# Kernel optimization log

Measured on AMD Instinct MI355X. Metric: run time of the kernel, lower is better.

The kernel has to match this reference:

```python
import jax, jax.numpy as jnp
import numpy as np

B, A, NN, G, F, L, MAXZ = 8, 1024, 64, 25, 128, 3, 100
CUTOFF = 5.0

def ssp(x):
    # shifted softplus: ln(0.5*e^x + 0.5) = softplus(x) - ln(2)
    return jax.nn.softplus(x) - jnp.log(2.0)

def setup_inputs() -> dict:
    key = jax.random.key(0)
    ks = jax.random.split(key, 10)
    atomic_numbers = jax.random.randint(ks[0], (B, A), 0, MAXZ)
    positions = jax.random.normal(ks[1], (B, A, 3), dtype=jnp.float32) * 3.0
    cell = jnp.zeros((B, 3, 3), dtype=jnp.float32)
    cell_offset = jnp.zeros((B, A, NN, 3), dtype=jnp.float32)
    neighbors = jax.random.randint(ks[2], (B, A, NN), 0, A)
    neighbor_mask = jnp.ones((B, A, NN), dtype=jnp.float32)
    s = 0.05
    emb = jax.random.normal(ks[3], (MAXZ, F), dtype=jnp.float32) * s
    emb = emb.at[0].set(0.0)  # padding_idx=0
    return dict(
        atomic_numbers=atomic_numbers, positions=positions, cell=cell,
        cell_offset=cell_offset, neighbors=neighbors, neighbor_mask=neighbor_mask,
        emb=emb,
        fw1=jax.random.normal(ks[4], (L, G, F), dtype=jnp.float32) * s,
        fb1=jnp.zeros((L, F), dtype=jnp.float32),
        fw2=jax.random.normal(ks[5], (L, F, F), dtype=jnp.float32) * s,
        fb2=jnp.zeros((L, F), dtype=jnp.float32),
        in2f_w=jax.random.normal(ks[6], (L, F, F), dtype=jnp.float32) * s,
        f2out_w=jax.random.normal(ks[7], (L, F, F), dtype=jnp.float32) * s,
        f2out_b=jnp.zeros((L, F), dtype=jnp.float32),
        dense_w=jax.random.normal(ks[8], (L, F, F), dtype=jnp.float32) * s,
        dense_b=jnp.zeros((L, F), dtype=jnp.float32),
    )

def reference(atomic_numbers, positions, cell, cell_offset, neighbors,
              neighbor_mask, emb, fw1, fb1, fw2, fb2, in2f_w, f2out_w,
              f2out_b, dense_w, dense_b):
    bidx = jnp.arange(B)[:, None, None]
    # embedding lookup [B,A,F]
    x = emb[atomic_numbers]
    # AtomDistances: gather neighbor positions, add cell offsets, norm
    pos_j = positions[bidx, neighbors]                       # [B,A,NN,3]
    dv = pos_j - positions[:, :, None, :] + jnp.einsum('bank,bkc->banc', cell_offset, cell)
    d2 = jnp.sum(dv * dv, axis=-1)                           # [B,A,NN]
    r_ij = jnp.where(d2 > 0, jnp.sqrt(jnp.where(d2 > 0, d2, 1.0)), 0.0)
    # GaussianSmearing on [0, cutoff] with G gaussians
    offsets = jnp.linspace(0.0, CUTOFF, G)
    width = offsets[1] - offsets[0]
    coeff = -0.5 / (width * width)
    f_ij = jnp.exp(coeff * (r_ij[..., None] - offsets) ** 2)  # [B,A,NN,G]
    mask = neighbor_mask[..., None]                           # [B,A,NN,1]
    for l in range(L):
        # filter-generating network on expanded distances -> [B,A,NN,F]
        W = ssp(f_ij @ fw1[l] + fb1[l]) @ fw2[l] + fb2[l]
        # cfconv: in2f (no bias), gather neighbor features, mul, masked sum
        y = x @ in2f_w[l]                                     # [B,A,F]
        yj = y[bidx, neighbors]                               # [B,A,NN,F]
        v = jnp.sum(yj * W * mask, axis=2)                    # [B,A,F]
        v = ssp(v @ f2out_w[l] + f2out_b[l])
        # interaction output dense (linear)
        v = v @ dense_w[l] + dense_b[l]
        x = x + v
    return x
```

## Files before the change

kernel.cpp:

```cpp
#include <hip/hip_runtime.h>
#include <hip/hip_bf16.h>
#include <math.h>

#define B_ 8
#define A_ 1024
#define NN_ 64
#define G_ 25
#define F_ 128
#define L_ 3
#define TG_ 4096
#define TGP_ (TG_ + 8)
#define SCT 32.0f
#define SCY 64.0f
#define INVS (1.0f/(32.0f*64.0f))

typedef __hip_bfloat16 bf16;
typedef __bf16 bf16x8 __attribute__((ext_vector_type(8)));
typedef __bf16 bf16x4 __attribute__((ext_vector_type(4)));
typedef float floatx4 __attribute__((ext_vector_type(4)));
typedef float floatx2 __attribute__((ext_vector_type(2)));
#define MFMA16 __builtin_amdgcn_mfma_f32_16x16x32_bf16
#define CVT8 __builtin_amdgcn_cvt_pk_f32_fp8

__device__ __forceinline__ float sspfast(float x){
  return __logf(0.5f*__expf(x) + 0.5f);
}
__device__ __forceinline__ float ldsel(const void* p, long long i, int isbf){
  return isbf ? __bfloat162float(((const bf16*)p)[i]) : ((const float*)p)[i];
}
__device__ __forceinline__ int sniff_bf16(const void* pos){
  const unsigned* raw = (const unsigned*)pos;
  unsigned w = raw[threadIdx.x & 63];
  unsigned e = (w >> 7) & 0xFF;
  return __popcll(__ballot(e >= 118 && e <= 132)) >= 32;
}
__device__ __forceinline__ unsigned int pack4_fp8(float a, float b, float c, float d){
  int r = __builtin_amdgcn_cvt_pk_fp8_f32(a, b, 0, false);
  r = __builtin_amdgcn_cvt_pk_fp8_f32(c, d, r, true);
  return (unsigned int)r;
}

__global__ __launch_bounds__(256) void k_setup(
    const void* emb, const void* fb1, const void* fb2, const void* f2ob,
    const void* db,  const void* fw1, const void* fw2, const void* f2ow,
    const void* dw,  const void* in2f, const void* pos,
    float* c_emb, float* c_fb1, float* c_fb2, float* c_f2ob, float* c_db,
    __bf16* fw1tb, __bf16* fw2tb, __bf16* f2owtb, __bf16* dwtb, __bf16* in2ftb)
{
  int isbf = sniff_bf16(pos);
  int idx = blockIdx.x*256 + threadIdx.x;
  if(idx < 12800){ c_emb[idx] = ldsel(emb, idx, isbf); return; }
  if(idx < 13184){ c_fb1[idx-12800] = ldsel(fb1, idx-12800, isbf); return; }
  if(idx < 13568){ c_fb2[idx-13184] = ldsel(fb2, idx-13184, isbf); return; }
  if(idx < 13952){ c_f2ob[idx-13568] = ldsel(f2ob, idx-13568, isbf); return; }
  if(idx < 14336){ c_db[idx-13952] = ldsel(db, idx-13952, isbf); return; }
  if(idx < 26624){
    int i = idx - 14336;
    int l = i >> 12; int rem = i & 4095; int f = rem >> 5; int k = rem & 31;
    float v = (k < G_) ? ldsel(fw1, (long long)l*G_*F_ + k*F_ + f, isbf) : 0.0f;
    fw1tb[i] = (__bf16)v;
    return;
  }
  {
    int i = idx - 26624;
    int which = i / 49152; int r = i - which*49152;
    int l = r >> 14; int rem = r & 16383; int f = rem >> 7; int k = rem & 127;
    const void* src = (which==0) ? fw2 : (which==1) ? f2ow : (which==2) ? dw : in2f;
    __bf16* dst = (which==0) ? fw2tb : (which==1) ? f2owtb : (which==2) ? dwtb : in2ftb;
    dst[r] = (__bf16)ldsel(src, (long long)l*F_*F_ + k*F_ + f, isbf);
  }
}

__global__ __launch_bounds__(256, 4) void k_build(
    const __bf16* __restrict__ fw1tb, const float* __restrict__ fb1g,
    const __bf16* __restrict__ fw2tb, const float* __restrict__ fb2g,
    unsigned char* __restrict__ wtab8,
    const int* __restrict__ z, const float* __restrict__ c_emb,
    const __bf16* __restrict__ in2ftb, float* __restrict__ xws,
    unsigned char* __restrict__ y8,
    const void* pos, const void* cell, const void* celloff,
    const int* __restrict__ nbr, const void* maskg,
    int2* __restrict__ pair)
{
  __shared__ __align__(16) unsigned char smem[22528];
  int t = threadIdx.x;
  int lane = t & 63, wid = t >> 6, c = lane & 15, quad = lane >> 4;
  int wb = wid*32;

  if(blockIdx.x >= 448){
    int isbf = sniff_bf16(pos);
    int p = (blockIdx.x - 448)*256 + t;
    int m = p >> 6;
    int b = m >> 10;
    int j = nbr[p];
    long long pi = (long long)m*3, pj = (long long)(b*A_+j)*3;
    long long co = (long long)p*3, ce = (long long)b*9;
    float o0 = ldsel(celloff,co+0,isbf), o1 = ldsel(celloff,co+1,isbf), o2 = ldsel(celloff,co+2,isbf);
    float d2 = 0.0f;
    #pragma unroll
    for(int cc=0;cc<3;cc++){
      float off = o0*ldsel(cell,ce+cc,isbf) + o1*ldsel(cell,ce+3+cc,isbf) + o2*ldsel(cell,ce+6+cc,isbf);
      float dv = ldsel(pos,pj+cc,isbf) - ldsel(pos,pi+cc,isbf) + off;
      d2 += dv*dv;
    }
    float r = (d2 > 0.0f) ? sqrtf(d2) : 0.0f;
    float msk = ldsel(maskg, p, isbf);
    int i = (int)(r * ((float)TG_ / 8.0f) + 0.5f);
    if(i > TG_-1) i = TG_-1;
    if(msk < 0.5f) i = TG_;
    int2 pr;
    pr.x = i * F_;
    pr.y = (b*A_ + j) * F_;
    pair[p] = pr;
    return;
  }

  if(blockIdx.x < 192){
    __bf16* s_h1  = (__bf16*)smem;
    __bf16* s_fij = (__bf16*)(smem + 17408);
    int layer = blockIdx.x >> 6;
    int row0  = (blockIdx.x & 63) * 64;
    unsigned char* T8 = wtab8 + (long long)layer*TGP_*F_;

    if((blockIdx.x & 63) == 0 && t < 32)
      *(unsigned int*)(T8 + (long long)TG_*F_ + t*4) = 0u;

    const float dr = 8.0f / (float)TG_;
    const float width = 5.0f/24.0f;
    const float coeff = -0.5f/(width*width);
    for(int i=t;i<NN_*40;i+=256){
      int n = i/40, g = i - n*40;
      float val = 0.0f;
      if(g < G_){
        float rg = (float)(row0 + n) * dr;
        float d = rg - (float)g*width;
        val = __expf(coeff*d*d);
      }
      s_fij[i] = (__bf16)val;
    }
    __syncthreads();

    {
      const __bf16* fw1l = fw1tb + layer*F_*32;
      bf16x8 a0 = *(const bf16x8*)(fw1l + (wb + c)*32 + quad*8);
      bf16x8 a1 = *(const bf16x8*)(fw1l + (wb + 16 + c)*32 + quad*8);
      floatx4 bias0 = *(const floatx4*)(fb1g + layer*F_ + wb + quad*4);
      floatx4 bias1 = *(const floatx4*)(fb1g + layer*F_ + wb + 16 + quad*4);
      #pragma unroll
      for(int nt=0;nt<4;nt++){
        bf16x8 bfr = *(const bf16x8*)(s_fij + (nt*16 + c)*40 + quad*8);
        floatx4 z4 = {0.f,0.f,0.f,0.f};
        floatx4 acc0 = MFMA16(a0, bfr, z4, 0,0,0);
        floatx4 acc1 = MFMA16(a1, bfr, z4, 0,0,0);
        bf16x4 h0, h1v;
        #pragma unroll
        for(int r=0;r<4;r++){
          h0[r]  = (__bf16)sspfast(acc0[r] + bias0[r]);
          h1v[r] = (__bf16)sspfast(acc1[r] + bias1[r]);
        }
        *(bf16x4*)(s_h1 + (nt*16+c)*136 + wb + quad*4)      = h0;
        *(bf16x4*)(s_h1 + (nt*16+c)*136 + wb + 16 + quad*4) = h1v;
      }
    }
    __syncthreads();

    {
      const __bf16* fw2l = fw2tb + layer*F_*F_;
      bf16x8 aw0[4], aw1[4];
      #pragma unroll
      for(int kt=0;kt<4;kt++){
        aw0[kt] = *(const bf16x8*)(fw2l + (wb + c)*F_ + kt*32 + quad*8);
        aw1[kt] = *(const bf16x8*)(fw2l + (wb + 16 + c)*F_ + kt*32 + quad*8);
      }
      floatx4 ba0 = *(const floatx4*)(fb2g + layer*F_ + wb + quad*4);
      floatx4 ba1 = *(const floatx4*)(fb2g + layer*F_ + wb + 16 + quad*4);
      #pragma unroll
      for(int nt=0; nt<4; nt++){
        bf16x8 bh[4];
        #pragma unroll
        for(int kt=0;kt<4;kt++)
          bh[kt] = *(const bf16x8*)(s_h1 + (nt*16 + c)*136 + kt*32 + quad*8);
        floatx4 acc0 = {0.f,0.f,0.f,0.f};
        floatx4 acc1 = {0.f,0.f,0.f,0.f};
        #pragma unroll
        for(int kt=0;kt<4;kt++){
          acc0 = MFMA16(aw0[kt], bh[kt], acc0, 0,0,0);
          acc1 = MFMA16(aw1[kt], bh[kt], acc1, 0,0,0);
        }
        int row = row0 + nt*16 + c;
        unsigned int w0 = pack4_fp8((acc0[0]+ba0[0])*SCT, (acc0[1]+ba0[1])*SCT,
                                    (acc0[2]+ba0[2])*SCT, (acc0[3]+ba0[3])*SCT);
        unsigned int w1 = pack4_fp8((acc1[0]+ba1[0])*SCT, (acc1[1]+ba1[1])*SCT,
                                    (acc1[2]+ba1[2])*SCT, (acc1[3]+ba1[3])*SCT);
        *(unsigned int*)(T8 + (long long)row*F_ + wb + quad*4)      = w0;
        *(unsigned int*)(T8 + (long long)row*F_ + wb + 16 + quad*4) = w1;
      }
    }
    return;
  }

  {
    __bf16* s_a = (__bf16*)smem;
    int row0 = (blockIdx.x - 192)*32;
    #pragma unroll
    for(int i=0;i<2;i++){
      int ch = t + i*256, row = ch >> 4, col8 = ch & 15;
      const float* src = c_emb + (long long)z[row0+row]*F_ + col8*8;
      float4 a4 = ((const float4*)src)[0];
      float4 b4 = ((const float4*)src)[1];
      float* xd = xws + (long long)(row0+row)*F_ + col8*8;
      ((float4*)xd)[0] = a4; ((float4*)xd)[1] = b4;
      bf16x8 v = {(__bf16)a4.x,(__bf16)a4.y,(__bf16)a4.z,(__bf16)a4.w,
                  (__bf16)b4.x,(__bf16)b4.y,(__bf16)b4.z,(__bf16)b4.w};
      *(bf16x8*)(s_a + row*136 + col8*8) = v;
    }
    __syncthreads();
    bf16x8 aw0[4], aw1[4];
    #pragma unroll
    for(int kt=0;kt<4;kt++){
      aw0[kt] = *(const bf16x8*)(in2ftb + (wb + c)*F_ + kt*32 + quad*8);
      aw1[kt] = *(const bf16x8*)(in2ftb + (wb + 16 + c)*F_ + kt*32 + quad*8);
    }
    #pragma unroll
    for(int nt=0; nt<2; nt++){
      bf16x8 bh[4];
      #pragma unroll
      for(int kt=0;kt<4;kt++)
        bh[kt] = *(const bf16x8*)(s_a + (nt*16 + c)*136 + kt*32 + quad*8);
      floatx4 acc0 = {0.f,0.f,0.f,0.f};
      floatx4 acc1 = {0.f,0.f,0.f,0.f};
      #pragma unroll
      for(int kt=0;kt<4;kt++){
        acc0 = MFMA16(aw0[kt], bh[kt], acc0, 0,0,0);
        acc1 = MFMA16(aw1[kt], bh[kt], acc1, 0,0,0);
      }
      int row = row0 + nt*16 + c;
      unsigned int w0 = pack4_fp8(acc0[0]*SCY, acc0[1]*SCY, acc0[2]*SCY, acc0[3]*SCY);
      unsigned int w1 = pack4_fp8(acc1[0]*SCY, acc1[1]*SCY, acc1[2]*SCY, acc1[3]*SCY);
      *(unsigned int*)(y8 + (long long)row*F_ + wb + quad*4)      = w0;
      *(unsigned int*)(y8 + (long long)row*F_ + wb + 16 + quad*4) = w1;
    }
  }
}

__global__ __launch_bounds__(512, 4) void k_layer(
    const unsigned char* __restrict__ yin, const int2* __restrict__ pairg,
    const unsigned char* __restrict__ Tb, float* __restrict__ xws,
    const __bf16* __restrict__ f2owl, const float* __restrict__ f2obl,
    const __bf16* __restrict__ dwl,  const float* __restrict__ dbl,
    const __bf16* __restrict__ in2fnext, unsigned char* __restrict__ yout,
    void* __restrict__ dout, const void* __restrict__ pos,
    int has_next, int write_out)
{
  __shared__ __align__(16) __bf16 s_ga[16*136];
  __shared__ __align__(16) __bf16 s_gb[16*136];

  int t = threadIdx.x;
  int bid = (int)blockIdx.x;
  int m0 = ((bid & 7) * 64 + (bid >> 3)) * 16;
  int lane = t & 63, wid = t >> 6, c = lane & 15, quad = lane >> 4;
  int isbf = sniff_bf16(pos);
  int wb = wid*16;

  int fs  = lane & 7;
  int grp = lane >> 3;
  int f16 = fs*16;

  const int2* pbase = pairg + (long long)m0*NN_;
  int2 prs0[8], prs1[8];
  {
    int a0 = wid*2, a1 = wid*2 + 1;
    #pragma unroll
    for(int jj=0; jj<8; jj++){
      prs0[jj] = pbase[a0*NN_ + jj*8 + grp];
      prs1[jj] = pbase[a1*NN_ + jj*8 + grp];
    }
  }

  #pragma unroll
  for(int aa=0; aa<2; aa++){
    int a = wid*2 + aa;
    float v0=0.f,v1=0.f,v2=0.f,v3=0.f,v4=0.f,v5=0.f,v6=0.f,v7=0.f;
    float v8=0.f,v9=0.f,v10=0.f,v11=0.f,v12=0.f,v13=0.f,v14=0.f,v15=0.f;
    #pragma unroll
    for(int jj=0; jj<8; jj++){
      int2 pr = aa ? prs1[jj] : prs0[jj];
      uint4 Tw = *(const uint4*)(Tb + pr.x + f16);
      uint4 Yw = *(const uint4*)(yin + pr.y + f16);
      floatx2 ta0 = CVT8((int)Tw.x,false), ta1 = CVT8((int)Tw.x,true);
      floatx2 ta2 = CVT8((int)Tw.y,false), ta3 = CVT8((int)Tw.y,true);
      floatx2 ta4 = CVT8((int)Tw.z,false), ta5 = CVT8((int)Tw.z,true);
      floatx2 ta6 = CVT8((int)Tw.w,false), ta7 = CVT8((int)Tw.w,true);
      floatx2 ua0 = CVT8((int)Yw.x,false), ua1 = CVT8((int)Yw.x,true);
      floatx2 ua2 = CVT8((int)Yw.y,false), ua3 = CVT8((int)Yw.y,true);
      floatx2 ua4 = CVT8((int)Yw.z,false), ua5 = CVT8((int)Yw.z,true);
      floatx2 ua6 = CVT8((int)Yw.w,false), ua7 = CVT8((int)Yw.w,true);
      v0  += ta0[0]*ua0[0];  v1  += ta0[1]*ua0[1];
      v2  += ta1[0]*ua1[0];  v3  += ta1[1]*ua1[1];
      v4  += ta2[0]*ua2[0];  v5  += ta2[1]*ua2[1];
      v6  += ta3[0]*ua3[0];  v7  += ta3[1]*ua3[1];
      v8  += ta4[0]*ua4[0];  v9  += ta4[1]*ua4[1];
      v10 += ta5[0]*ua5[0];  v11 += ta5[1]*ua5[1];
      v12 += ta6[0]*ua6[0];  v13 += ta6[1]*ua6[1];
      v14 += ta7[0]*ua7[0];  v15 += ta7[1]*ua7[1];
    }
    #define RED(m) \
      v0 += __shfl_xor(v0,m);  v1 += __shfl_xor(v1,m);  v2 += __shfl_xor(v2,m);  v3 += __shfl_xor(v3,m); \
      v4 += __shfl_xor(v4,m);  v5 += __shfl_xor(v5,m);  v6 += __shfl_xor(v6,m);  v7 += __shfl_xor(v7,m); \
      v8 += __shfl_xor(v8,m);  v9 += __shfl_xor(v9,m);  v10 += __shfl_xor(v10,m); v11 += __shfl_xor(v11,m); \
      v12 += __shfl_xor(v12,m); v13 += __shfl_xor(v13,m); v14 += __shfl_xor(v14,m); v15 += __shfl_xor(v15,m);
    RED(8) RED(16) RED(32)
    #undef RED
    if(lane < 8){
      bf16x8 o0 = {(__bf16)(v0*INVS),(__bf16)(v1*INVS),(__bf16)(v2*INVS),(__bf16)(v3*INVS),
                   (__bf16)(v4*INVS),(__bf16)(v5*INVS),(__bf16)(v6*INVS),(__bf16)(v7*INVS)};
      bf16x8 o1 = {(__bf16)(v8*INVS),(__bf16)(v9*INVS),(__bf16)(v10*INVS),(__bf16)(v11*INVS),
                   (__bf16)(v12*INVS),(__bf16)(v13*INVS),(__bf16)(v14*INVS),(__bf16)(v15*INVS)};
      *(bf16x8*)(s_ga + a*136 + fs*16)     = o0;
      *(bf16x8*)(s_ga + a*136 + fs*16 + 8) = o1;
    }
  }
  __syncthreads();

  {
    bf16x8 aw[4];
    #pragma unroll
    for(int kt=0;kt<4;kt++)
      aw[kt] = *(const bf16x8*)(f2owl + (wb + c)*F_ + kt*32 + quad*8);
    floatx4 ba = *(const floatx4*)(f2obl + wb + quad*4);
    bf16x8 bh[4];
    #pragma unroll
    for(int kt=0;kt<4;kt++)
      bh[kt] = *(const bf16x8*)(s_ga + c*136 + kt*32 + quad*8);
    floatx4 acc = {0.f,0.f,0.f,0.f};
    #pragma unroll
    for(int kt=0;kt<4;kt++)
      acc = MFMA16(aw[kt], bh[kt], acc, 0,0,0);
    bf16x4 o;
    #pragma unroll
    for(int r=0;r<4;r++)
      o[r] = (__bf16)sspfast(acc[r] + ba[r]);
    *(bf16x4*)(s_gb + c*136 + wb + quad*4) = o;
  }
  __syncthreads();

  {
    bf16x8 aw[4];
    #pragma unroll
    for(int kt=0;kt<4;kt++)
      aw[kt] = *(const bf16x8*)(dwl + (wb + c)*F_ + kt*32 + quad*8);
    floatx4 ba = *(const floatx4*)(dbl + wb + quad*4);
    bf16x8 bh[4];
    #pragma unroll
    for(int kt=0;kt<4;kt++)
      bh[kt] = *(const bf16x8*)(s_gb + c*136 + kt*32 + quad*8);
    floatx4 acc = {0.f,0.f,0.f,0.f};
    #pragma unroll
    for(int kt=0;kt<4;kt++)
      acc = MFMA16(aw[kt], bh[kt], acc, 0,0,0);
    int rowL = m0 + c;
    float* xp = xws + (long long)rowL*F_ + wb + quad*4;
    float4 x0 = *(const float4*)xp;
    float4 xn = {x0.x+acc[0]+ba[0], x0.y+acc[1]+ba[1],
                 x0.z+acc[2]+ba[2], x0.w+acc[3]+ba[3]};
    bf16x4 s0 = {(__bf16)xn.x,(__bf16)xn.y,(__bf16)xn.z,(__bf16)xn.w};
    *(bf16x4*)(s_ga + c*136 + wb + quad*4) = s0;
    *(float4*)xp = xn;
    if(write_out){
      long long gi = (long long)rowL*F_ + wb + quad*4;
      if(isbf){
        *(bf16x4*)((bf16*)dout + gi) = s0;
      }else{
        *(float4*)((float*)dout + gi) = xn;
      }
    }
  }
  if(!has_next) return;
  __syncthreads();

  {
    bf16x8 aw[4];
    #pragma unroll
    for(int kt=0;kt<4;kt++)
      aw[kt] = *(const bf16x8*)(in2fnext + (wb + c)*F_ + kt*32 + quad*8);
    bf16x8 bh[4];
    #pragma unroll
    for(int kt=0;kt<4;kt++)
      bh[kt] = *(const bf16x8*)(s_ga + c*136 + kt*32 + quad*8);
    floatx4 acc = {0.f,0.f,0.f,0.f};
    #pragma unroll
    for(int kt=0;kt<4;kt++)
      acc = MFMA16(aw[kt], bh[kt], acc, 0,0,0);
    int row = m0 + c;
    unsigned int w0 = pack4_fp8(acc[0]*SCY, acc[1]*SCY, acc[2]*SCY, acc[3]*SCY);
    *(unsigned int*)(yout + (long long)row*F_ + wb + quad*4) = w0;
  }
}

extern "C" void kernel_launch(void* const* d_in, const int* in_sizes, int n_in,
                              void* d_out, int out_size, void* d_ws, size_t ws_size,
                              hipStream_t stream){
  const int*  z       = (const int*)d_in[0];
  const void* pos     = d_in[1];
  const void* cell    = d_in[2];
  const void* celloff = d_in[3];
  const int*  nbr     = (const int*)d_in[4];
  const void* mask    = d_in[5];
  const void* emb     = d_in[6];
  const void* fw1     = d_in[7];
  const void* fb1     = d_in[8];
  const void* fw2     = d_in[9];
  const void* fb2     = d_in[10];
  const void* in2f    = d_in[11];
  const void* f2ow    = d_in[12];
  const void* f2ob    = d_in[13];
  const void* dw      = d_in[14];
  const void* db      = d_in[15];

  float* base = (float*)d_ws;
  float* c_emb  = base + 16;
  float* c_fb1  = c_emb + 12800;
  float* c_fb2  = c_fb1 + 384;
  float* c_f2ob = c_fb2 + 384;
  float* c_db   = c_f2ob + 384;
  __bf16* fw1tb  = (__bf16*)(c_db + 384);
  __bf16* fw2tb  = (__bf16*)(base + 20496);
  __bf16* f2owtb = (__bf16*)(base + 45072);
  __bf16* dwtb   = (__bf16*)(base + 69648);
  __bf16* in2ftb = (__bf16*)(base + 94224);
  float*  xws   = base + 118800;
  unsigned char* y8_0 = (unsigned char*)(base + 1167376);
  unsigned char* y8_1 = (unsigned char*)(base + 1429520);
  int2*   pair  = (int2*)(base + 1691664);
  unsigned char* wtab8 = (unsigned char*)(base + 2740240);

  k_setup<<<872, 256, 0, stream>>>(emb, fb1, fb2, f2ob, db,
                                   fw1, fw2, f2ow, dw, in2f, pos,
                                   c_emb, c_fb1, c_fb2, c_f2ob, c_db,
                                   fw1tb, fw2tb, f2owtb, dwtb, in2ftb);
  k_build<<<2496, 256, 0, stream>>>(fw1tb, c_fb1, fw2tb, c_fb2, wtab8,
                                    z, c_emb, in2ftb, xws, y8_0,
                                    pos, cell, celloff, nbr, mask, pair);

  unsigned char* ycur = y8_0;
  unsigned char* ynext = y8_1;
  for(int l=0;l<L_;l++){
    k_layer<<<(B_*A_)/16, 512, 0, stream>>>(ycur, pair,
                                            wtab8 + (long long)l*TGP_*F_, xws,
                                            f2owtb + l*F_*F_, c_f2ob + l*F_,
                                            dwtb + l*F_*F_,  c_db + l*F_,
                                            in2ftb + (l < L_-1 ? (l+1)*F_*F_ : 0), ynext,
                                            d_out, pos,
                                            (l < L_-1) ? 1 : 0, (l == L_-1) ? 1 : 0);
    unsigned char* tmp = ycur; ycur = ynext; ynext = tmp;
  }
}
```

Measured before the change: 155.2 us.

## Fold setup kernel into build kernel, reading raw weights directly

Removes the separate k_setup launch and moves its work into k_build. The table-build and embedding blocks now read fw1/fw2/fb/emb/in2f straight from the raw inputs with per-element dtype conversion, and new trailing blocks transpose f2ow/dw/in2f and copy the biases for the later layer kernels. Block order is rearranged so the pair-distance blocks come first. This removes one launch and its serialization, at the cost of uncoalesced strided scalar weight loads in each table/embedding block. The embedding-stage in2f load now reads raw layer-0 weights instead of the transposed buffer, which the fused kernel fills concurrently.

Result: slower. 169.0 us (+8.9%).

```diff
diff --git a/kernel.cpp b/kernel.cpp
--- a/kernel.cpp
+++ b/kernel.cpp
@@ -40,56 +40,27 @@
   return (unsigned int)r;
 }
 
-__global__ __launch_bounds__(256) void k_setup(
-    const void* emb, const void* fb1, const void* fb2, const void* f2ob,
-    const void* db,  const void* fw1, const void* fw2, const void* f2ow,
-    const void* dw,  const void* in2f, const void* pos,
-    float* c_emb, float* c_fb1, float* c_fb2, float* c_f2ob, float* c_db,
-    __bf16* fw1tb, __bf16* fw2tb, __bf16* f2owtb, __bf16* dwtb, __bf16* in2ftb)
-{
-  int isbf = sniff_bf16(pos);
-  int idx = blockIdx.x*256 + threadIdx.x;
-  if(idx < 12800){ c_emb[idx] = ldsel(emb, idx, isbf); return; }
-  if(idx < 13184){ c_fb1[idx-12800] = ldsel(fb1, idx-12800, isbf); return; }
-  if(idx < 13568){ c_fb2[idx-13184] = ldsel(fb2, idx-13184, isbf); return; }
-  if(idx < 13952){ c_f2ob[idx-13568] = ldsel(f2ob, idx-13568, isbf); return; }
-  if(idx < 14336){ c_db[idx-13952] = ldsel(db, idx-13952, isbf); return; }
-  if(idx < 26624){
-    int i = idx - 14336;
-    int l = i >> 12; int rem = i & 4095; int f = rem >> 5; int k = rem & 31;
-    float v = (k < G_) ? ldsel(fw1, (long long)l*G_*F_ + k*F_ + f, isbf) : 0.0f;
-    fw1tb[i] = (__bf16)v;
-    return;
-  }
-  {
-    int i = idx - 26624;
-    int which = i / 49152; int r = i - which*49152;
-    int l = r >> 14; int rem = r & 16383; int f = rem >> 7; int k = rem & 127;
-    const void* src = (which==0) ? fw2 : (which==1) ? f2ow : (which==2) ? dw : in2f;
-    __bf16* dst = (which==0) ? fw2tb : (which==1) ? f2owtb : (which==2) ? dwtb : in2ftb;
-    dst[r] = (__bf16)ldsel(src, (long long)l*F_*F_ + k*F_ + f, isbf);
-  }
-}
-
 __global__ __launch_bounds__(256, 4) void k_build(
-    const __bf16* __restrict__ fw1tb, const float* __restrict__ fb1g,
-    const __bf16* __restrict__ fw2tb, const float* __restrict__ fb2g,
-    unsigned char* __restrict__ wtab8,
-    const int* __restrict__ z, const float* __restrict__ c_emb,
-    const __bf16* __restrict__ in2ftb, float* __restrict__ xws,
-    unsigned char* __restrict__ y8,
     const void* pos, const void* cell, const void* celloff,
     const int* __restrict__ nbr, const void* maskg,
-    int2* __restrict__ pair)
+    const void* emb, const void* fw1, const void* fb1, const void* fw2,
+    const void* fb2, const void* in2f, const void* f2ow, const void* f2ob,
+    const void* dw, const void* db, const int* __restrict__ z,
+    unsigned char* __restrict__ wtab8, float* __restrict__ xws,
+    unsigned char* __restrict__ y8, int2* __restrict__ pair,
+    __bf16* __restrict__ f2owtb, __bf16* __restrict__ dwtb,
+    __bf16* __restrict__ in2ftb, float* __restrict__ c_f2ob,
+    float* __restrict__ c_db)
 {
   __shared__ __align__(16) unsigned char smem[22528];
   int t = threadIdx.x;
+  int bid = (int)blockIdx.x;
   int lane = t & 63, wid = t >> 6, c = lane & 15, quad = lane >> 4;
   int wb = wid*32;
 
-  if(blockIdx.x >= 448){
+  if(bid < 2048){
     int isbf = sniff_bf16(pos);
-    int p = (blockIdx.x - 448)*256 + t;
+    int p = bid*256 + t;
     int m = p >> 6;
     int b = m >> 10;
     int j = nbr[p];
@@ -115,15 +86,43 @@
     return;
   }
 
-  if(blockIdx.x < 192){
+  if(bid < 2240){
     __bf16* s_h1  = (__bf16*)smem;
     __bf16* s_fij = (__bf16*)(smem + 17408);
-    int layer = blockIdx.x >> 6;
-    int row0  = (blockIdx.x & 63) * 64;
+    int isbf = sniff_bf16(pos);
+    int tb = bid - 2048;
+    int layer = tb >> 6;
+    int row0  = (tb & 63) * 64;
     unsigned char* T8 = wtab8 + (long long)layer*TGP_*F_;
 
-    if((blockIdx.x & 63) == 0 && t < 32)
+    if((tb & 63) == 0 && t < 32)
       *(unsigned int*)(T8 + (long long)TG_*F_ + t*4) = 0u;
+
+    bf16x8 a0, a1;
+    #pragma unroll
+    for(int e=0;e<8;e++){
+      int k = quad*8 + e;
+      a0[e] = (__bf16)((k < G_) ? ldsel(fw1,(long long)layer*G_*F_ + k*F_ + (wb+c), isbf) : 0.0f);
+      a1[e] = (__bf16)((k < G_) ? ldsel(fw1,(long long)layer*G_*F_ + k*F_ + (wb+16+c), isbf) : 0.0f);
+    }
+    float bb10[4], bb11[4], bb20[4], bb21[4];
+    #pragma unroll
+    for(int r=0;r<4;r++){
+      bb10[r] = ldsel(fb1, (long long)layer*F_ + wb + quad*4 + r, isbf);
+      bb11[r] = ldsel(fb1, (long long)layer*F_ + wb + 16 + quad*4 + r, isbf);
+      bb20[r] = ldsel(fb2, (long long)layer*F_ + wb + quad*4 + r, isbf);
+      bb21[r] = ldsel(fb2, (long long)layer*F_ + wb + 16 + quad*4 + r, isbf);
+    }
+    bf16x8 aw0[4], aw1[4];
+    #pragma unroll
+    for(int kt=0;kt<4;kt++){
+      #pragma unroll
+      for(int e=0;e<8;e++){
+        int k = kt*32 + quad*8 + e;
+        aw0[kt][e] = (__bf16)ldsel(fw2,(long long)layer*F_*F_ + k*F_ + (wb+c), isbf);
+        aw1[kt][e] = (__bf16)ldsel(fw2,(long long)layer*F_*F_ + k*F_ + (wb+16+c), isbf);
+      }
+    }
 
     const float dr = 8.0f / (float)TG_;
     const float width = 5.0f/24.0f;
@@ -141,11 +140,6 @@
     __syncthreads();
 
     {
-      const __bf16* fw1l = fw1tb + layer*F_*32;
-      bf16x8 a0 = *(const bf16x8*)(fw1l + (wb + c)*32 + quad*8);
-      bf16x8 a1 = *(const bf16x8*)(fw1l + (wb + 16 + c)*32 + quad*8);
-      floatx4 bias0 = *(const floatx4*)(fb1g + layer*F_ + wb + quad*4);
-      floatx4 bias1 = *(const floatx4*)(fb1g + layer*F_ + wb + 16 + quad*4);
       #pragma unroll
       for(int nt=0;nt<4;nt++){
         bf16x8 bfr = *(const bf16x8*)(s_fij + (nt*16 + c)*40 + quad*8);
@@ -155,8 +149,8 @@
         bf16x4 h0, h1v;
         #pragma unroll
         for(int r=0;r<4;r++){
-          h0[r]  = (__bf16)sspfast(acc0[r] + bias0[r]);
-          h1v[r] = (__bf16)sspfast(acc1[r] + bias1[r]);
+          h0[r]  = (__bf16)sspfast(acc0[r] + bb10[r]);
+          h1v[r] = (__bf16)sspfast(acc1[r] + bb11[r]);
         }
         *(bf16x4*)(s_h1 + (nt*16+c)*136 + wb + quad*4)      = h0;
         *(bf16x4*)(s_h1 + (nt*16+c)*136 + wb + 16 + quad*4) = h1v;
@@ -165,15 +159,6 @@
     __syncthreads();
 
     {
-      const __bf16* fw2l = fw2tb + layer*F_*F_;
-      bf16x8 aw0[4], aw1[4];
-      #pragma unroll
-      for(int kt=0;kt<4;kt++){
-        aw0[kt] = *(const bf16x8*)(fw2l + (wb + c)*F_ + kt*32 + quad*8);
-        aw1[kt] = *(const bf16x8*)(fw2l + (wb + 16 + c)*F_ + kt*32 + quad*8);
-      }
-      floatx4 ba0 = *(const floatx4*)(fb2g + layer*F_ + wb + quad*4);
-      floatx4 ba1 = *(const floatx4*)(fb2g + layer*F_ + wb + 16 + quad*4);
       #pragma unroll
       for(int nt=0; nt<4; nt++){
         bf16x8 bh[4];
@@ -188,10 +173,10 @@
           acc1 = MFMA16(aw1[kt], bh[kt], acc1, 0,0,0);
         }
         int row = row0 + nt*16 + c;
-        unsigned int w0 = pack4_fp8((acc0[0]+ba0[0])*SCT, (acc0[1]+ba0[1])*SCT,
-                                    (acc0[2]+ba0[2])*SCT, (acc0[3]+ba0[3])*SCT);
-        unsigned int w1 = pack4_fp8((acc1[0]+ba1[0])*SCT, (acc1[1]+ba1[1])*SCT,
-                                    (acc1[2]+ba1[2])*SCT, (acc1[3]+ba1[3])*SCT);
+        unsigned int w0 = pack4_fp8((acc0[0]+bb20[0])*SCT, (acc0[1]+bb20[1])*SCT,
+                                    (acc0[2]+bb20[2])*SCT, (acc0[3]+bb20[3])*SCT);
+        unsigned int w1 = pack4_fp8((acc1[0]+bb21[0])*SCT, (acc1[1]+bb21[1])*SCT,
+                                    (acc1[2]+bb21[2])*SCT, (acc1[3]+bb21[3])*SCT);
         *(unsigned int*)(T8 + (long long)row*F_ + wb + quad*4)      = w0;
         *(unsigned int*)(T8 + (long long)row*F_ + wb + 16 + quad*4) = w1;
       }
@@ -199,28 +184,35 @@
     return;
   }
 
-  {
+  if(bid < 2496){
     __bf16* s_a = (__bf16*)smem;
-    int row0 = (blockIdx.x - 192)*32;
+    int isbf = sniff_bf16(pos);
+    int row0 = (bid - 2240)*32;
     #pragma unroll
     for(int i=0;i<2;i++){
       int ch = t + i*256, row = ch >> 4, col8 = ch & 15;
-      const float* src = c_emb + (long long)z[row0+row]*F_ + col8*8;
-      float4 a4 = ((const float4*)src)[0];
-      float4 b4 = ((const float4*)src)[1];
+      long long zb = (long long)z[row0+row]*F_ + col8*8;
+      float v[8];
+      #pragma unroll
+      for(int e=0;e<8;e++) v[e] = ldsel(emb, zb + e, isbf);
       float* xd = xws + (long long)(row0+row)*F_ + col8*8;
-      ((float4*)xd)[0] = a4; ((float4*)xd)[1] = b4;
-      bf16x8 v = {(__bf16)a4.x,(__bf16)a4.y,(__bf16)a4.z,(__bf16)a4.w,
-                  (__bf16)b4.x,(__bf16)b4.y,(__bf16)b4.z,(__bf16)b4.w};
-      *(bf16x8*)(s_a + row*136 + col8*8) = v;
+      ((float4*)xd)[0] = make_float4(v[0],v[1],v[2],v[3]);
+      ((float4*)xd)[1] = make_float4(v[4],v[5],v[6],v[7]);
+      bf16x8 bv = {(__bf16)v[0],(__bf16)v[1],(__bf16)v[2],(__bf16)v[3],
+                   (__bf16)v[4],(__bf16)v[5],(__bf16)v[6],(__bf16)v[7]};
+      *(bf16x8*)(s_a + row*136 + col8*8) = bv;
+    }
+    bf16x8 aw0[4], aw1[4];
+    #pragma unroll
+    for(int kt=0;kt<4;kt++){
+      #pragma unroll
+      for(int e=0;e<8;e++){
+        int k = kt*32 + quad*8 + e;
+        aw0[kt][e] = (__bf16)ldsel(in2f,(long long)k*F_ + (wb+c), isbf);
+        aw1[kt][e] = (__bf16)ldsel(in2f,(long long)k*F_ + (wb+16+c), isbf);
+      }
     }
     __syncthreads();
-    bf16x8 aw0[4], aw1[4];
-    #pragma unroll
-    for(int kt=0;kt<4;kt++){
-      aw0[kt] = *(const bf16x8*)(in2ftb + (wb + c)*F_ + kt*32 + quad*8);
-      aw1[kt] = *(const bf16x8*)(in2ftb + (wb + 16 + c)*F_ + kt*32 + quad*8);
-    }
     #pragma unroll
     for(int nt=0; nt<2; nt++){
       bf16x8 bh[4];
@@ -240,6 +232,24 @@
       *(unsigned int*)(y8 + (long long)row*F_ + wb + quad*4)      = w0;
       *(unsigned int*)(y8 + (long long)row*F_ + wb + 16 + quad*4) = w1;
     }
+    return;
+  }
+
+  if(bid < 3072){
+    int isbf = sniff_bf16(pos);
+    int i = (bid - 2496)*256 + t;
+    int which = i / 49152; int r = i - which*49152;
+    int l = r >> 14; int rem = r & 16383; int f = rem >> 7; int k = rem & 127;
+    const void* src = (which==0) ? f2ow : (which==1) ? dw : in2f;
+    __bf16* dst = (which==0) ? f2owtb : (which==1) ? dwtb : in2ftb;
+    dst[r] = (__bf16)ldsel(src, (long long)l*F_*F_ + k*F_ + f, isbf);
+    return;
+  }
+  {
+    int isbf = sniff_bf16(pos);
+    int i = (bid - 3072)*256 + t;
+    if(i < 384)      c_f2ob[i] = ldsel(f2ob, i, isbf);
+    else if(i < 768) c_db[i-384] = ldsel(db, i-384, isbf);
   }
 }
 
@@ -418,13 +428,8 @@
   const void* db      = d_in[15];
 
   float* base = (float*)d_ws;
-  float* c_emb  = base + 16;
-  float* c_fb1  = c_emb + 12800;
-  float* c_fb2  = c_fb1 + 384;
-  float* c_f2ob = c_fb2 + 384;
+  float* c_f2ob = base + 16;
   float* c_db   = c_f2ob + 384;
-  __bf16* fw1tb  = (__bf16*)(c_db + 384);
-  __bf16* fw2tb  = (__bf16*)(base + 20496);
   __bf16* f2owtb = (__bf16*)(base + 45072);
   __bf16* dwtb   = (__bf16*)(base + 69648);
   __bf16* in2ftb = (__bf16*)(base + 94224);
@@ -434,13 +439,11 @@
   int2*   pair  = (int2*)(base + 1691664);
   unsigned char* wtab8 = (unsigned char*)(base + 2740240);
 
-  k_setup<<<872, 256, 0, stream>>>(emb, fb1, fb2, f2ob, db,
-                                   fw1, fw2, f2ow, dw, in2f, pos,
-                                   c_emb, c_fb1, c_fb2, c_f2ob, c_db,
-                                   fw1tb, fw2tb, f2owtb, dwtb, in2ftb);
-  k_build<<<2496, 256, 0, stream>>>(fw1tb, c_fb1, fw2tb, c_fb2, wtab8,
-                                    z, c_emb, in2ftb, xws, y8_0,
-                                    pos, cell, celloff, nbr, mask, pair);
+  k_build<<<3075, 256, 0, stream>>>(pos, cell, celloff, nbr, mask,
+                                    emb, fw1, fb1, fw2, fb2, in2f,
+                                    f2ow, f2ob, dw, db, z,
+                                    wtab8, xws, y8_0, pair,
+                                    f2owtb, dwtb, in2ftb, c_f2ob, c_db);
 
   unsigned char* ycur = y8_0;
   unsigned char* ynext = y8_1;
```
